# Kernel optimization log

Measured on AMD Instinct MI355X. Metric: run time of the kernel, lower is better.

The kernel has to match this reference:

```python
import jax, jax.numpy as jnp
import numpy as np

TAU = 2.0      # LIF membrane time constant
VTH = 1.0      # spiking threshold (spikingjelly default)
ALPHA = 4.0    # surrogate sigmoid sharpness (spikingjelly Sigmoid default)
EPS = 1e-5     # BatchNorm eps


@jax.custom_vjp
def spike(v):
    # Heaviside(v) with surrogate sigmoid gradient
    return (v >= 0.0).astype(v.dtype)

def _spike_fwd(v):
    return spike(v), v

def _spike_bwd(v, g):
    s = jax.nn.sigmoid(ALPHA * v)
    return (g * ALPHA * s * (1.0 - s),)

spike.defvjp(_spike_fwd, _spike_bwd)


def lif(x_seq):
    # MultiStepLIFNode: x_seq [T, B, C], v_reset=0 (hard reset), detach_reset=True
    def step(v, xt):
        v = v + (xt - v) / TAU           # membrane decay + charge
        s = spike(v - VTH)               # fire
        v = v * (1.0 - jax.lax.stop_gradient(s))  # detached hard reset to 0
        return v, s
    v0 = jnp.zeros_like(x_seq[0])
    _, s_seq = jax.lax.scan(step, v0, x_seq)
    return s_seq


def block(h, w, b, gamma, beta):
    # h: [B, C_in, T] -> conv1d(k=3, pad=1) -> BN (batch stats) -> LIF -> [B, E, T]
    y = jax.lax.conv_general_dilated(h, w, window_strides=(1,), padding=[(1, 1)],
                                     dimension_numbers=('NCH', 'OIH', 'NCH'))
    y = y + b[None, :, None]
    mu = y.mean(axis=(0, 2), keepdims=True)
    var = y.var(axis=(0, 2), keepdims=True)
    y = (y - mu) * jax.lax.rsqrt(var + EPS) * gamma[None, :, None] + beta[None, :, None]
    s = lif(jnp.transpose(y, (2, 0, 1)))        # [T, B, E]
    return jnp.transpose(s, (1, 2, 0))          # [B, E, T]


def setup_inputs() -> dict:
    key = jax.random.key(0)
    ks = jax.random.split(key, 8)
    B, T, Cin, E, O = 64, 1024, 8, 256, 63
    return {
        'x':       jax.random.normal(ks[0], (B, T, Cin), jnp.float32),
        'conv0_w': jax.random.normal(ks[1], (E, Cin, 3), jnp.float32) * (1.0 / np.sqrt(Cin * 3)),
        'conv0_b': jax.random.normal(ks[2], (E,), jnp.float32) * 0.01,
        'convs_w': jax.random.normal(ks[3], (3, E, E, 3), jnp.float32) * (1.0 / np.sqrt(E * 3)),
        'convs_b': jax.random.normal(ks[4], (3, E), jnp.float32) * 0.01,
        'bn_gamma': jnp.ones((4, E), jnp.float32),
        'bn_beta':  jnp.zeros((4, E), jnp.float32),
        'head_w':  jax.random.normal(ks[5], (O, E), jnp.float32) * (1.0 / np.sqrt(E)),
        'head_b':  jnp.zeros((O,), jnp.float32),
    }


def reference(x, conv0_w, conv0_b, convs_w, convs_b, bn_gamma, bn_beta, head_w, head_b):
    h = jnp.transpose(x, (0, 2, 1))  # [B, C, T]
    h = block(h, conv0_w, conv0_b, bn_gamma[0], bn_beta[0])
    for i in range(convs_w.shape[0]):
        h = block(h, convs_w[i], convs_b[i], bn_gamma[i + 1], bn_beta[i + 1])
    h = h.mean(axis=-1)  # AdaptiveAvgPool1d(1) + squeeze -> [B, E]
    return h @ head_w.T + head_b  # [B, O]
```

## Files before the change

kernel.cpp:

```cpp
#include <hip/hip_runtime.h>
#include <hip/hip_bf16.h>
#include <stdint.h>

#define NB 64
#define NT 1024
#define CIN 8
#define NE 256
#define NO 63
#define TPAD 16
#define TROWS (NT + 2*TPAD)
#define LCH 128
#define LWU 48
#define TT 256

using bf16x8 = __attribute__((ext_vector_type(8))) short;
using f32x4  = __attribute__((ext_vector_type(4))) float;
typedef unsigned int u32;


__global__ void conv0_prep(const float* __restrict__ x, const float* __restrict__ w0,
                           const float* __restrict__ b0, float* __restrict__ y,
                           double* __restrict__ acc0,
                           const float* __restrict__ cw, __hip_bfloat16* __restrict__ wfr) {
    int bid = blockIdx.x;
    if (bid >= 512) {
        int F = (bid - 512) * 256 + threadIdx.x;
        int lane = F & 63;
        int xx = F >> 6;
        int cph = xx & 7;  xx >>= 3;
        int e4  = xx & 15; xx >>= 4;
        int s   = xx & 1;  xx >>= 1;
        int k   = xx % 3;
        int l   = xx / 3;
        int e = e4*16 + (lane & 15);
        int cb = cph*32 + (lane >> 4)*8;
        __hip_bfloat16 outv[8];
        #pragma unroll
        for (int j = 0; j < 8; ++j) {
            float w = cw[((size_t)(l*256 + e)*256 + (cb + j))*3 + k];
            __hip_bfloat16 hi = __float2bfloat16(w);
            if (s == 0) outv[j] = hi;
            else        outv[j] = __float2bfloat16(w - __bfloat162float(hi));
        }
        *(uint4*)(wfr + (size_t)F*8) = *(uint4*)outv;
        return;
    }
    int b = bid >> 3, tc = bid & 7;
    int e = threadIdx.x;
    int t0 = tc * 128;
    __shared__ float xs[1040];
    for (int i = threadIdx.x; i < 1040; i += 256) {
        int t = t0 - 1 + (i >> 3); int c = i & 7;
        xs[i] = (t >= 0 && t < NT) ? x[((size_t)b*NT + t)*CIN + c] : 0.0f;
    }
    __syncthreads();
    float w[24];
    #pragma unroll
    for (int j = 0; j < 24; ++j) w[j] = w0[e*24 + j];
    float bias = b0[e];
    float s = 0.0f, qq = 0.0f;
    for (int dt = 0; dt < 128; ++dt) {
        float acc = bias;
        #pragma unroll
        for (int c = 0; c < 8; ++c)
            #pragma unroll
            for (int k = 0; k < 3; ++k)
                acc += xs[(dt + k)*8 + c] * w[c*3 + k];
        y[((size_t)b*NT + t0 + dt)*NE + e] = acc;
        s += acc; qq += acc*acc;
    }
    atomicAdd(&acc0[e],       (double)s);
    atomicAdd(&acc0[256 + e], (double)qq);
}

template<bool WS>
__global__ void lif_kern(const float* __restrict__ y, const double* __restrict__ acc,
                         const float* __restrict__ gamma, const float* __restrict__ beta,
                         __hip_bfloat16* __restrict__ S, float* __restrict__ pool) {
    int c = blockIdx.x, b = blockIdx.y;
    int e = threadIdx.x;
    double sa = acc[e], qa = acc[256 + e];
    double mean = sa * (1.0/65536.0);
    double var  = qa * (1.0/65536.0) - mean*mean;
    float rs  = (float)(1.0 / sqrt(var + 1e-5));
    float mu  = (float)mean;
    float rsg = rs * gamma[e];
    float bet = beta[e];
    const __hip_bfloat16 z   = __float2bfloat16(0.0f);
    const __hip_bfloat16 one = __float2bfloat16(1.0f);
    if (WS) {
        if (c == 0) {
            for (int r = 0; r < TPAD; ++r) S[((size_t)b*TROWS + r)*NE + e] = z;
        }
        if (c == 7) {
            for (int r = 0; r < TPAD; ++r) S[((size_t)b*TROWS + TPAD + NT + r)*NE + e] = z;
        }
    }
    int t0 = c * LCH;
    int tw = t0 - LWU; if (tw < 0) tw = 0;
    const float* yb = y + (size_t)b*NT*NE + e;
    __hip_bfloat16* sb = S + ((size_t)b*TROWS + TPAD)*NE + e;
    float v = 0.0f;
    #pragma unroll 8
    for (int t = tw; t < t0; ++t) {
        float xx = yb[(size_t)t*NE];
        float yn = (xx - mu)*rsg + bet;
        float d  = __fsub_rn(yn, v);
        v = __fadd_rn(v, __fmul_rn(d, 0.5f));
        v = (v >= 1.0f) ? 0.0f : v;
    }
    float cnt = 0.0f;
    #pragma unroll 8
    for (int t = t0; t < t0 + LCH; ++t) {
        float xx = yb[(size_t)t*NE];
        float yn = (xx - mu)*rsg + bet;
        float d  = __fsub_rn(yn, v);
        v = __fadd_rn(v, __fmul_rn(d, 0.5f));
        bool sp = (v >= 1.0f);
        if (WS) sb[(size_t)t*NE] = sp ? one : z;
        else    cnt += sp ? 1.0f : 0.0f;
        v = sp ? 0.0f : v;
    }
    if (!WS) pool[(size_t)(b*8 + c)*256 + e] = cnt;
}

__global__ __launch_bounds__(256, 4) void conv_mfma(
    const __hip_bfloat16* __restrict__ Sp,
    const __hip_bfloat16* __restrict__ Wfr,
    const float* __restrict__ bias,
    float* __restrict__ y,
    double* __restrict__ acc_out)
{
    __shared__ short Bbuf[2][272*32];
    const int tid  = threadIdx.x;
    const int wave = tid >> 6, lane = tid & 63;
    const int n16  = lane & 15, q = lane >> 4;
    const int we = wave & 1, wt = wave >> 1;
    const int flat = blockIdx.x;
    const int vid  = (flat & 7) * 128 + (flat >> 3);
    const int et = vid & 3, tt = (vid >> 2) & 3, b = vid >> 4;
    const int t0 = tt * TT;

    f32x4 acc[2][8] = {};

    const __hip_bfloat16* Sbase = Sp + ((size_t)b*TROWS + (TPAD - 1 + t0)) * NE;

    auto stage = [&](int buf, int c0) {
        for (int ch = wave; ch < 17; ch += 4) {
            int r  = ch*16 + (lane >> 2);
            int sg = (lane & 3) ^ ((r >> 1) & 3);
            const __hip_bfloat16* src = Sbase + (size_t)r*NE + c0 + sg*8;
            char* dst = (char*)(&Bbuf[0][0]) + buf*17408 + ch*1024;
            __builtin_amdgcn_global_load_lds(
                (const __attribute__((address_space(1))) u32*)src,
                (__attribute__((address_space(3))) u32*)dst, 16, 0, 0);
        }
    };

    stage(0, 0);
    asm volatile("s_waitcnt vmcnt(0)" ::: "memory");
    __syncthreads();

    for (int ph = 0; ph < 8; ++ph) {
        const int buf = ph & 1;
        const short* Bb = &Bbuf[buf][0];
        #pragma unroll 1
        for (int kk = 0; kk < 3; ++kk) {
            bf16x8 afr[2][2];
            #pragma unroll
            for (int s = 0; s < 2; ++s)
                #pragma unroll
                for (int f = 0; f < 2; ++f)
                    afr[s][f] = *(const bf16x8*)(Wfr +
                        ((((size_t)(kk*2 + s)*16 + et*4 + we*2 + f)*8 + ph) << 9) + lane*8);
            __builtin_amdgcn_sched_barrier(0);
            if (kk == 0 && ph < 7) stage(buf ^ 1, (ph + 1) * 32);
            __builtin_amdgcn_sched_barrier(0);
            __builtin_amdgcn_s_setprio(1);
            #pragma unroll
            for (int g = 0; g < 8; ++g) {
                int row = wt*128 + g*16 + n16 + kk;
                int sgs = q ^ ((row >> 1) & 3);
                bf16x8 bfr = *(const bf16x8*)((const char*)Bb + row*64 + sgs*16);
                #pragma unroll
                for (int s = 0; s < 2; ++s)
                    #pragma unroll
                    for (int f = 0; f < 2; ++f)
                        acc[f][g] = __builtin_amdgcn_mfma_f32_16x16x32_bf16(afr[s][f], bfr, acc[f][g], 0, 0, 0);
            }
            __builtin_amdgcn_s_setprio(0);
        }
        __builtin_amdgcn_s_barrier();
        __builtin_amdgcn_sched_barrier(0);
    }

    float ls[8], lq[8];
    #pragma unroll
    for (int f = 0; f < 2; ++f) {
        int e_loc = et*64 + we*32 + f*16 + q*4;
        float4 bv = *(const float4*)(bias + e_loc);
        float s0=0,s1=0,s2=0,s3=0, q0=0,q1=0,q2=0,q3=0;
        #pragma unroll
        for (int g = 0; g < 8; ++g) {
            int t = t0 + wt*128 + g*16 + n16;
            f32x4 a = acc[f][g];
            float4 o;
            o.x = a[0] + bv.x; o.y = a[1] + bv.y; o.z = a[2] + bv.z; o.w = a[3] + bv.w;
            *(float4*)(y + ((size_t)b*NT + t)*NE + e_loc) = o;
            s0 += o.x; q0 += o.x*o.x;
            s1 += o.y; q1 += o.y*o.y;
            s2 += o.z; q2 += o.z*o.z;
            s3 += o.w; q3 += o.w*o.w;
        }
        ls[f*4+0]=s0; lq[f*4+0]=q0;
        ls[f*4+1]=s1; lq[f*4+1]=q1;
        ls[f*4+2]=s2; lq[f*4+2]=q2;
        ls[f*4+3]=s3; lq[f*4+3]=q3;
    }
    #pragma unroll
    for (int off = 1; off < 16; off <<= 1) {
        #pragma unroll
        for (int i = 0; i < 8; ++i) {
            ls[i] += __shfl_xor(ls[i], off, 64);
            lq[i] += __shfl_xor(lq[i], off, 64);
        }
    }
    __syncthreads();
    float* red = (float*)(&Bbuf[0][0]);
    if (n16 == 0 && wt == 0) {
        #pragma unroll
        for (int f = 0; f < 2; ++f)
            #pragma unroll
            for (int r = 0; r < 4; ++r) {
                int el = we*32 + f*16 + q*4 + r;
                red[el] = ls[f*4+r]; red[64+el] = lq[f*4+r];
            }
    }
    __syncthreads();
    if (n16 == 0 && wt == 1) {
        #pragma unroll
        for (int f = 0; f < 2; ++f)
            #pragma unroll
            for (int r = 0; r < 4; ++r) {
                int el = we*32 + f*16 + q*4 + r;
                red[el] += ls[f*4+r]; red[64+el] += lq[f*4+r];
            }
    }
    __syncthreads();
    if (tid < 64) {
        int e = et*64 + tid;
        atomicAdd(&acc_out[e],       (double)red[tid]);
        atomicAdd(&acc_out[256 + e], (double)red[64 + tid]);
    }
}

__global__ void head_final(const float* __restrict__ pool, const float* __restrict__ hw,
                           const float* __restrict__ hb, float* __restrict__ out) {
    int b = blockIdx.x;
    int tid = threadIdx.x;
    __shared__ float pooled[256];
    float s = 0.0f;
    #pragma unroll
    for (int c = 0; c < 8; ++c) s += pool[(size_t)(b*8 + c)*256 + tid];
    pooled[tid] = s * (1.0f/1024.0f);
    __syncthreads();
    if (tid < NO) {
        float acc = hb[tid];
        for (int c = 0; c < 256; ++c) acc += pooled[c] * hw[tid*256 + c];
        out[b*NO + tid] = acc;
    }
}

extern "C" void kernel_launch(void* const* d_in, const int* in_sizes, int n_in,
                              void* d_out, int out_size, void* d_ws, size_t ws_size,
                              hipStream_t stream) {
    (void)in_sizes; (void)n_in; (void)out_size; (void)ws_size;
    const float* x       = (const float*)d_in[0];
    const float* conv0_w = (const float*)d_in[1];
    const float* conv0_b = (const float*)d_in[2];
    const float* convs_w = (const float*)d_in[3];
    const float* convs_b = (const float*)d_in[4];
    const float* bn_g    = (const float*)d_in[5];
    const float* bn_b    = (const float*)d_in[6];
    const float* head_w  = (const float*)d_in[7];
    const float* head_b  = (const float*)d_in[8];
    float* out = (float*)d_out;

    char* ws = (char*)d_ws;
    float*          y    = (float*)ws;
    __hip_bfloat16* S    = (__hip_bfloat16*)(ws + 67108864);
    __hip_bfloat16* Wfr  = (__hip_bfloat16*)(ws + 101711872);
    double*         acc  = (double*)(ws + 104071168);
    float*          pool = (float*)(ws + 104087552);

    conv0_prep<<<1088, 256, 0, stream>>>(x, conv0_w, conv0_b, y, acc, convs_w, Wfr);
    lif_kern<true><<<dim3(8, 64), 256, 0, stream>>>(y, acc, bn_g, bn_b, S, nullptr);

    for (int l = 0; l < 3; ++l) {
        conv_mfma<<<1024, 256, 0, stream>>>(S, Wfr + (size_t)l*393216,
                                            convs_b + l*256, y, acc + (l+1)*512);
        const float* g = bn_g + (l+1)*256;
        const float* bb = bn_b + (l+1)*256;
        if (l < 2) lif_kern<true ><<<dim3(8, 64), 256, 0, stream>>>(y, acc + (l+1)*512, g, bb, S, nullptr);
        else       lif_kern<false><<<dim3(8, 64), 256, 0, stream>>>(y, acc + (l+1)*512, g, bb, S, pool);
    }
    head_final<<<64, 256, 0, stream>>>(pool, head_w, head_b, out);
}
```

Baseline: 310.5 us.

## Halve conv time tile and give each wave 16 channels to raise occupancy

The conv kernel's time tile shrinks from 256 to 128 and the grid doubles to 2048 blocks. Each wave now computes 16 output channels over 128 time steps instead of 32 channels over 128 steps within a 2x2 wave layout. This halves the accumulator registers and the LDS buffer so launch bounds can allow 8 blocks per CU. The LDS cross-wave reduction is replaced by direct per-wave double atomics. In exchange, each B fragment read from LDS now feeds fewer MFMAs, halo staging is duplicated more often, and there are more global atomics.

```diff
diff --git a/kernel.cpp b/kernel.cpp
--- a/kernel.cpp
+++ b/kernel.cpp
@@ -11,7 +11,7 @@
 #define TROWS (NT + 2*TPAD)
 #define LCH 128
 #define LWU 48
-#define TT 256
+#define TT 128
 
 using bf16x8 = __attribute__((ext_vector_type(8))) short;
 using f32x4  = __attribute__((ext_vector_type(4))) float;
@@ -124,33 +124,32 @@
     if (!WS) pool[(size_t)(b*8 + c)*256 + e] = cnt;
 }
 
-__global__ __launch_bounds__(256, 4) void conv_mfma(
+__global__ __launch_bounds__(256, 8) void conv_mfma(
     const __hip_bfloat16* __restrict__ Sp,
     const __hip_bfloat16* __restrict__ Wfr,
     const float* __restrict__ bias,
     float* __restrict__ y,
     double* __restrict__ acc_out)
 {
-    __shared__ short Bbuf[2][272*32];
+    __shared__ short Bbuf[2][144*32];
     const int tid  = threadIdx.x;
     const int wave = tid >> 6, lane = tid & 63;
     const int n16  = lane & 15, q = lane >> 4;
-    const int we = wave & 1, wt = wave >> 1;
     const int flat = blockIdx.x;
-    const int vid  = (flat & 7) * 128 + (flat >> 3);
-    const int et = vid & 3, tt = (vid >> 2) & 3, b = vid >> 4;
+    const int vid  = (flat & 7) * 256 + (flat >> 3);
+    const int et = vid & 3, tt = (vid >> 2) & 7, b = vid >> 5;
     const int t0 = tt * TT;
 
-    f32x4 acc[2][8] = {};
+    f32x4 acc[8] = {};
 
     const __hip_bfloat16* Sbase = Sp + ((size_t)b*TROWS + (TPAD - 1 + t0)) * NE;
 
     auto stage = [&](int buf, int c0) {
-        for (int ch = wave; ch < 17; ch += 4) {
+        for (int ch = wave; ch < 9; ch += 4) {
             int r  = ch*16 + (lane >> 2);
             int sg = (lane & 3) ^ ((r >> 1) & 3);
             const __hip_bfloat16* src = Sbase + (size_t)r*NE + c0 + sg*8;
-            char* dst = (char*)(&Bbuf[0][0]) + buf*17408 + ch*1024;
+            char* dst = (char*)(&Bbuf[0][0]) + buf*9216 + ch*1024;
             __builtin_amdgcn_global_load_lds(
                 (const __attribute__((address_space(1))) u32*)src,
                 (__attribute__((address_space(3))) u32*)dst, 16, 0, 0);
@@ -166,27 +165,22 @@
         const short* Bb = &Bbuf[buf][0];
         #pragma unroll 1
         for (int kk = 0; kk < 3; ++kk) {
-            bf16x8 afr[2][2];
+            bf16x8 afr[2];
             #pragma unroll
             for (int s = 0; s < 2; ++s)
-                #pragma unroll
-                for (int f = 0; f < 2; ++f)
-                    afr[s][f] = *(const bf16x8*)(Wfr +
-                        ((((size_t)(kk*2 + s)*16 + et*4 + we*2 + f)*8 + ph) << 9) + lane*8);
+                afr[s] = *(const bf16x8*)(Wfr +
+                    ((((size_t)(kk*2 + s)*16 + et*4 + wave)*8 + ph) << 9) + lane*8);
             __builtin_amdgcn_sched_barrier(0);
             if (kk == 0 && ph < 7) stage(buf ^ 1, (ph + 1) * 32);
             __builtin_amdgcn_sched_barrier(0);
             __builtin_amdgcn_s_setprio(1);
             #pragma unroll
             for (int g = 0; g < 8; ++g) {
-                int row = wt*128 + g*16 + n16 + kk;
+                int row = g*16 + n16 + kk;
                 int sgs = q ^ ((row >> 1) & 3);
                 bf16x8 bfr = *(const bf16x8*)((const char*)Bb + row*64 + sgs*16);
-                #pragma unroll
-                for (int s = 0; s < 2; ++s)
-                    #pragma unroll
-                    for (int f = 0; f < 2; ++f)
-                        acc[f][g] = __builtin_amdgcn_mfma_f32_16x16x32_bf16(afr[s][f], bfr, acc[f][g], 0, 0, 0);
+                acc[g] = __builtin_amdgcn_mfma_f32_16x16x32_bf16(afr[0], bfr, acc[g], 0, 0, 0);
+                acc[g] = __builtin_amdgcn_mfma_f32_16x16x32_bf16(afr[1], bfr, acc[g], 0, 0, 0);
             }
             __builtin_amdgcn_s_setprio(0);
         }
@@ -194,63 +188,35 @@
         __builtin_amdgcn_sched_barrier(0);
     }
 
-    float ls[8], lq[8];
-    #pragma unroll
-    for (int f = 0; f < 2; ++f) {
-        int e_loc = et*64 + we*32 + f*16 + q*4;
-        float4 bv = *(const float4*)(bias + e_loc);
-        float s0=0,s1=0,s2=0,s3=0, q0=0,q1=0,q2=0,q3=0;
-        #pragma unroll
-        for (int g = 0; g < 8; ++g) {
-            int t = t0 + wt*128 + g*16 + n16;
-            f32x4 a = acc[f][g];
-            float4 o;
-            o.x = a[0] + bv.x; o.y = a[1] + bv.y; o.z = a[2] + bv.z; o.w = a[3] + bv.w;
-            *(float4*)(y + ((size_t)b*NT + t)*NE + e_loc) = o;
-            s0 += o.x; q0 += o.x*o.x;
-            s1 += o.y; q1 += o.y*o.y;
-            s2 += o.z; q2 += o.z*o.z;
-            s3 += o.w; q3 += o.w*o.w;
-        }
-        ls[f*4+0]=s0; lq[f*4+0]=q0;
-        ls[f*4+1]=s1; lq[f*4+1]=q1;
-        ls[f*4+2]=s2; lq[f*4+2]=q2;
-        ls[f*4+3]=s3; lq[f*4+3]=q3;
+    const int e_loc = et*64 + wave*16 + q*4;
+    float4 bv = *(const float4*)(bias + e_loc);
+    float ls[4] = {0,0,0,0}, lq[4] = {0,0,0,0};
+    #pragma unroll
+    for (int g = 0; g < 8; ++g) {
+        int t = t0 + g*16 + n16;
+        f32x4 a = acc[g];
+        float4 o;
+        o.x = a[0] + bv.x; o.y = a[1] + bv.y; o.z = a[2] + bv.z; o.w = a[3] + bv.w;
+        *(float4*)(y + ((size_t)b*NT + t)*NE + e_loc) = o;
+        ls[0] += o.x; lq[0] += o.x*o.x;
+        ls[1] += o.y; lq[1] += o.y*o.y;
+        ls[2] += o.z; lq[2] += o.z*o.z;
+        ls[3] += o.w; lq[3] += o.w*o.w;
     }
     #pragma unroll
     for (int off = 1; off < 16; off <<= 1) {
         #pragma unroll
-        for (int i = 0; i < 8; ++i) {
+        for (int i = 0; i < 4; ++i) {
             ls[i] += __shfl_xor(ls[i], off, 64);
             lq[i] += __shfl_xor(lq[i], off, 64);
         }
     }
-    __syncthreads();
-    float* red = (float*)(&Bbuf[0][0]);
-    if (n16 == 0 && wt == 0) {
-        #pragma unroll
-        for (int f = 0; f < 2; ++f)
-            #pragma unroll
-            for (int r = 0; r < 4; ++r) {
-                int el = we*32 + f*16 + q*4 + r;
-                red[el] = ls[f*4+r]; red[64+el] = lq[f*4+r];
-            }
-    }
-    __syncthreads();
-    if (n16 == 0 && wt == 1) {
-        #pragma unroll
-        for (int f = 0; f < 2; ++f)
-            #pragma unroll
-            for (int r = 0; r < 4; ++r) {
-                int el = we*32 + f*16 + q*4 + r;
-                red[el] += ls[f*4+r]; red[64+el] += lq[f*4+r];
-            }
-    }
-    __syncthreads();
-    if (tid < 64) {
-        int e = et*64 + tid;
-        atomicAdd(&acc_out[e],       (double)red[tid]);
-        atomicAdd(&acc_out[256 + e], (double)red[64 + tid]);
+    if (n16 == 0) {
+        #pragma unroll
+        for (int r = 0; r < 4; ++r) {
+            atomicAdd(&acc_out[e_loc + r],       (double)ls[r]);
+            atomicAdd(&acc_out[256 + e_loc + r], (double)lq[r]);
+        }
     }
 }
 
@@ -297,7 +263,7 @@
     lif_kern<true><<<dim3(8, 64), 256, 0, stream>>>(y, acc, bn_g, bn_b, S, nullptr);
 
     for (int l = 0; l < 3; ++l) {
-        conv_mfma<<<1024, 256, 0, stream>>>(S, Wfr + (size_t)l*393216,
+        conv_mfma<<<2048, 256, 0, stream>>>(S, Wfr + (size_t)l*393216,
                                             convs_b + l*256, y, acc + (l+1)*512);
         const float* g = bn_g + (l+1)*256;
         const float* bb = bn_b + (l+1)*256;
```

Result: slower. 395.1 us (+27.3%).

## Halve conv time tile to 128 rows with 2-wave blocks and direct atomics

Applied to the files above, without the earlier changes.

Splits the conv GEMM into twice as many blocks, each covering 128 time steps with two waves instead of 256 steps with four, shrinking shared staging buffers accordingly. The cross-wave LDS reduction of BatchNorm statistics is replaced with direct per-lane double atomics to global memory. The LIF warmup length is also reduced from 48 to 40 steps. This aims to raise occupancy and drop block-level barriers, at the cost of more halo re-reads, more weight-fragment loads per output, and more atomic traffic on the statistics buffer.

```diff
diff --git a/kernel.cpp b/kernel.cpp
--- a/kernel.cpp
+++ b/kernel.cpp
@@ -10,8 +10,8 @@
 #define TPAD 16
 #define TROWS (NT + 2*TPAD)
 #define LCH 128
-#define LWU 48
-#define TT 256
+#define LWU 40
+#define TT 128
 
 using bf16x8 = __attribute__((ext_vector_type(8))) short;
 using f32x4  = __attribute__((ext_vector_type(4))) float;
@@ -124,21 +124,20 @@
     if (!WS) pool[(size_t)(b*8 + c)*256 + e] = cnt;
 }
 
-__global__ __launch_bounds__(256, 4) void conv_mfma(
+__global__ __launch_bounds__(128, 4) void conv_mfma(
     const __hip_bfloat16* __restrict__ Sp,
     const __hip_bfloat16* __restrict__ Wfr,
     const float* __restrict__ bias,
     float* __restrict__ y,
     double* __restrict__ acc_out)
 {
-    __shared__ short Bbuf[2][272*32];
+    __shared__ short Bbuf[2][144*32];
     const int tid  = threadIdx.x;
-    const int wave = tid >> 6, lane = tid & 63;
+    const int we   = tid >> 6, lane = tid & 63;
     const int n16  = lane & 15, q = lane >> 4;
-    const int we = wave & 1, wt = wave >> 1;
     const int flat = blockIdx.x;
-    const int vid  = (flat & 7) * 128 + (flat >> 3);
-    const int et = vid & 3, tt = (vid >> 2) & 3, b = vid >> 4;
+    const int vid  = (flat & 7) * 256 + (flat >> 3);
+    const int et = vid & 3, tt = (vid >> 2) & 7, b = vid >> 5;
     const int t0 = tt * TT;
 
     f32x4 acc[2][8] = {};
@@ -146,11 +145,11 @@
     const __hip_bfloat16* Sbase = Sp + ((size_t)b*TROWS + (TPAD - 1 + t0)) * NE;
 
     auto stage = [&](int buf, int c0) {
-        for (int ch = wave; ch < 17; ch += 4) {
+        for (int ch = we; ch < 9; ch += 2) {
             int r  = ch*16 + (lane >> 2);
             int sg = (lane & 3) ^ ((r >> 1) & 3);
             const __hip_bfloat16* src = Sbase + (size_t)r*NE + c0 + sg*8;
-            char* dst = (char*)(&Bbuf[0][0]) + buf*17408 + ch*1024;
+            char* dst = (char*)(&Bbuf[0][0]) + buf*9216 + ch*1024;
             __builtin_amdgcn_global_load_lds(
                 (const __attribute__((address_space(1))) u32*)src,
                 (__attribute__((address_space(3))) u32*)dst, 16, 0, 0);
@@ -179,7 +178,7 @@
             __builtin_amdgcn_s_setprio(1);
             #pragma unroll
             for (int g = 0; g < 8; ++g) {
-                int row = wt*128 + g*16 + n16 + kk;
+                int row = g*16 + n16 + kk;
                 int sgs = q ^ ((row >> 1) & 3);
                 bf16x8 bfr = *(const bf16x8*)((const char*)Bb + row*64 + sgs*16);
                 #pragma unroll
@@ -202,7 +201,7 @@
         float s0=0,s1=0,s2=0,s3=0, q0=0,q1=0,q2=0,q3=0;
         #pragma unroll
         for (int g = 0; g < 8; ++g) {
-            int t = t0 + wt*128 + g*16 + n16;
+            int t = t0 + g*16 + n16;
             f32x4 a = acc[f][g];
             float4 o;
             o.x = a[0] + bv.x; o.y = a[1] + bv.y; o.z = a[2] + bv.z; o.w = a[3] + bv.w;
@@ -225,32 +224,16 @@
             lq[i] += __shfl_xor(lq[i], off, 64);
         }
     }
-    __syncthreads();
-    float* red = (float*)(&Bbuf[0][0]);
-    if (n16 == 0 && wt == 0) {
-        #pragma unroll
-        for (int f = 0; f < 2; ++f)
+    if (n16 == 0) {
+        #pragma unroll
+        for (int f = 0; f < 2; ++f) {
+            int e_loc = et*64 + we*32 + f*16 + q*4;
             #pragma unroll
             for (int r = 0; r < 4; ++r) {
-                int el = we*32 + f*16 + q*4 + r;
-                red[el] = ls[f*4+r]; red[64+el] = lq[f*4+r];
+                atomicAdd(&acc_out[e_loc + r],       (double)ls[f*4+r]);
+                atomicAdd(&acc_out[256 + e_loc + r], (double)lq[f*4+r]);
             }
-    }
-    __syncthreads();
-    if (n16 == 0 && wt == 1) {
-        #pragma unroll
-        for (int f = 0; f < 2; ++f)
-            #pragma unroll
-            for (int r = 0; r < 4; ++r) {
-                int el = we*32 + f*16 + q*4 + r;
-                red[el] += ls[f*4+r]; red[64+el] += lq[f*4+r];
-            }
-    }
-    __syncthreads();
-    if (tid < 64) {
-        int e = et*64 + tid;
-        atomicAdd(&acc_out[e],       (double)red[tid]);
-        atomicAdd(&acc_out[256 + e], (double)red[64 + tid]);
+        }
     }
 }
 
@@ -297,7 +280,7 @@
     lif_kern<true><<<dim3(8, 64), 256, 0, stream>>>(y, acc, bn_g, bn_b, S, nullptr);
 
     for (int l = 0; l < 3; ++l) {
-        conv_mfma<<<1024, 256, 0, stream>>>(S, Wfr + (size_t)l*393216,
+        conv_mfma<<<2048, 128, 0, stream>>>(S, Wfr + (size_t)l*393216,
                                             convs_b + l*256, y, acc + (l+1)*512);
         const float* g = bn_g + (l+1)*256;
         const float* bb = bn_b + (l+1)*256;
```

Result: slower. 399.3 us (+28.6%).
